# Performance work log

Measured on AMD Instinct MI355X. Metric: run time of the kernel, lower is better.

## Reference

```python
import jax, jax.numpy as jnp
import numpy as np

B, T, D = 2, 2048, 2048
H, KV, HD = 16, 8, 128
N_REP = H // KV
EPS = 1e-6
ROPE_THETA = 5e6
K_MASK = float(jnp.finfo(jnp.bfloat16).min)


def setup_inputs() -> dict:
    key = jax.random.key(0)
    ks = jax.random.split(key, 8)
    x = jax.random.normal(ks[0], (B, T, D), dtype=jnp.float32)
    wq = jax.random.normal(ks[1], (D, H * HD), dtype=jnp.float32) * 0.02
    wk = jax.random.normal(ks[2], (D, KV * HD), dtype=jnp.float32) * 0.02
    wv = jax.random.normal(ks[3], (D, KV * HD), dtype=jnp.float32) * 0.02
    wo = jax.random.normal(ks[4], (H * HD, D), dtype=jnp.float32) * 0.02
    qn_w = jnp.ones((HD,), dtype=jnp.float32)
    kn_w = jnp.ones((HD,), dtype=jnp.float32)
    # real rotary angles: [T, HD//2] -> broadcast to [B, T, HD//2]
    pos = jnp.arange(T, dtype=jnp.float32)
    inv_freq = 1.0 / (ROPE_THETA ** (jnp.arange(0, HD, 2, dtype=jnp.float32) / HD))
    ang = pos[:, None] * inv_freq[None, :]
    sin = jnp.broadcast_to(jnp.sin(ang)[None], (B, T, HD // 2))
    cos = jnp.broadcast_to(jnp.cos(ang)[None], (B, T, HD // 2))
    # causal mask [B, 1, T, T]
    causal = jnp.tril(jnp.ones((T, T), dtype=jnp.bool_))
    mask = jnp.broadcast_to(causal[None, None], (B, 1, T, T))
    k_cache = jnp.zeros((B, T, KV, HD), dtype=jnp.float32)
    v_cache = jnp.zeros((B, T, KV, HD), dtype=jnp.float32)
    return {"x": x, "wq": wq, "wk": wk, "wv": wv, "wo": wo,
            "qn_w": qn_w, "kn_w": kn_w, "sin": sin, "cos": cos,
            "mask": mask, "k_cache": k_cache, "v_cache": v_cache}


def _rms_norm(h, w):
    h32 = h.astype(jnp.float32)
    rms = jax.lax.rsqrt(jnp.mean(h32 * h32, axis=-1, keepdims=True) + EPS)
    return (h32 * rms * w).astype(h.dtype)


def _apply_rope(x, sin, cos):
    x1, x2 = x[..., : HD // 2], x[..., HD // 2:]
    s, c = sin[:, :, None, :], cos[:, :, None, :]  # [B,T,1,HD/2]
    return jnp.concatenate([x1 * c - x2 * s, x2 * c + x1 * s], axis=-1).astype(x.dtype)


def reference(x, wq, wk, wv, wo, qn_w, kn_w, sin, cos, mask, k_cache, v_cache):
    b, t, _ = x.shape
    q = _rms_norm((x @ wq).reshape(b, t, H, HD), qn_w)
    k = _rms_norm((x @ wk).reshape(b, t, KV, HD), kn_w)
    v = (x @ wv).reshape(b, t, KV, HD)
    q = _apply_rope(q, sin, cos)
    k = _apply_rope(k, sin, cos)
    # KV-cache update at cur_ind = 0 (prefill)
    k_cache = jax.lax.dynamic_update_slice(k_cache, k.astype(k_cache.dtype), (0, 0, 0, 0))
    v_cache = jax.lax.dynamic_update_slice(v_cache, v.astype(v_cache.dtype), (0, 0, 0, 0))
    # GQA repeat_kv: [B,S,KV,HD] -> [B,S,H,HD]
    kf = jnp.repeat(k_cache, N_REP, axis=2)
    vf = jnp.repeat(v_cache, N_REP, axis=2)
    scale = HD ** -0.5
    # [B,H,T,S]
    attn = jnp.einsum('bthd,bshd->bhts', q, kf) * scale
    attn = jnp.where(mask, attn, K_MASK)
    attn = jax.nn.softmax(attn.astype(jnp.float32), axis=-1).astype(q.dtype)
    out = jnp.einsum('bhts,bshd->bthd', attn, vf).reshape(b, t, H * HD)
    return out @ wo
```

## Files before the change

kernel.cpp:

```cpp
#include <hip/hip_runtime.h>
#include <hip/hip_bf16.h>
#include <stdint.h>

#define BB 2
#define TT 2048
#define DD 2048
#define HH 16
#define KVH 8
#define HDIM 128
#define BT (BB*TT)
#define NQKV (HH*HDIM + 2*KVH*HDIM)
#define TQ (TT/128)
#define ATT_SCALE 0.08838834764831845f
#define RMS_EPS 1e-6f

typedef __bf16 bf16;
typedef __bf16 bf16x8 __attribute__((ext_vector_type(8)));
typedef __bf16 bf16x4 __attribute__((ext_vector_type(4)));
typedef __bf16 bf16x2 __attribute__((ext_vector_type(2)));
typedef float  f32x4  __attribute__((ext_vector_type(4)));
typedef float  f32x16 __attribute__((ext_vector_type(16)));
typedef unsigned u32x4 __attribute__((ext_vector_type(4)));

__device__ __forceinline__ void gl_lds16(const void* g, const void* l) {
  __builtin_amdgcn_global_load_lds(
      (const __attribute__((address_space(1))) void*)(uintptr_t)g,
      (__attribute__((address_space(3))) void*)(uint32_t)(uintptr_t)l,
      16, 0, 0);
}

__device__ __forceinline__ unsigned pkbf(float lo, float hi) {
  bf16x2 t = { (bf16)lo, (bf16)hi };
  return __builtin_bit_cast(unsigned, t);
}

__global__ __launch_bounds__(256) void cast_bf16_k(const float* __restrict__ in,
                                                   bf16* __restrict__ out, int n4) {
  int i = blockIdx.x * blockDim.x + threadIdx.x;
  int stride = gridDim.x * blockDim.x;
  for (; i < n4; i += stride) {
    float4 v = ((const float4*)in)[i];
    bf16x4 o = { (bf16)v.x, (bf16)v.y, (bf16)v.z, (bf16)v.w };
    *(bf16x4*)(out + (size_t)i * 4) = o;
  }
}

__global__ __launch_bounds__(256) void transpose_cast_k(const float* __restrict__ in,
                                                        bf16* __restrict__ out,
                                                        int R, int C) {
  __shared__ float tile[32][33];
  int tx = threadIdx.x & 31, ty = threadIdx.x >> 5;
  int c0 = blockIdx.x * 32, r0 = blockIdx.y * 32;
#pragma unroll
  for (int i = 0; i < 4; ++i)
    tile[ty + 8*i][tx] = in[(size_t)(r0 + ty + 8*i) * C + c0 + tx];
  __syncthreads();
#pragma unroll
  for (int i = 0; i < 4; ++i)
    out[(size_t)(c0 + ty + 8*i) * R + r0 + tx] = (bf16)tile[tx][ty + 8*i];
}

__global__ __launch_bounds__(256) void transpose_v_k(const bf16* __restrict__ vb,
                                                     bf16* __restrict__ vbt) {
  __shared__ bf16 tile[32][33];
  int tx = threadIdx.x & 31, ty = threadIdx.x >> 5;
  int t0 = blockIdx.x * 32;
  int d0 = blockIdx.y * 32;
  int bk = blockIdx.z;
  int b = bk >> 3, kv = bk & 7;
#pragma unroll
  for (int i = 0; i < 4; ++i)
    tile[ty + 8*i][tx] = vb[(((size_t)(b*TT + t0 + ty + 8*i)) * KVH + kv) * HDIM + d0 + tx];
  __syncthreads();
#pragma unroll
  for (int i = 0; i < 4; ++i)
    vbt[(((size_t)bk) * HDIM + d0 + ty + 8*i) * TT + t0 + tx] = tile[tx][ty + 8*i];
}

template <int OUT_F32>
__global__ __launch_bounds__(256, 2)
void gemm_bt_k(const bf16* __restrict__ A, const bf16* __restrict__ Bt,
               void* __restrict__ Cout, int M, int N, int K) {
  __shared__ bf16 As[128 * 32];
  __shared__ bf16 Bs[128 * 32];
  const int tid = threadIdx.x;
  const int lane = tid & 63, wid = tid >> 6;
  const int lr = lane & 15, lq = lane >> 4;
  const int bm = blockIdx.y * 128, bn = blockIdx.x * 128;
  const int wr = wid >> 1, wc = wid & 1;
  const bf16* Ab = A + (size_t)bm * K;
  const bf16* Bb = Bt + (size_t)bn * K;
  f32x4 acc[4][4] = {};
  for (int k0 = 0; k0 < K; k0 += 32) {
#pragma unroll
    for (int r = 0; r < 2; ++r) {
      int ch = r * 256 + tid;
      int row = ch >> 2, c8 = ch & 3;
      const bf16* lbase = As + (size_t)(r * 256 + wid * 64) * 8;
      gl_lds16(Ab + (size_t)row * K + k0 + c8 * 8, lbase);
      const bf16* lbase2 = Bs + (size_t)(r * 256 + wid * 64) * 8;
      gl_lds16(Bb + (size_t)row * K + k0 + c8 * 8, lbase2);
    }
    __syncthreads();
    bf16x8 af[4], bfv[4];
#pragma unroll
    for (int m = 0; m < 4; ++m)
      af[m] = *(const bf16x8*)&As[(wr * 64 + m * 16 + lr) * 32 + lq * 8];
#pragma unroll
    for (int n = 0; n < 4; ++n)
      bfv[n] = *(const bf16x8*)&Bs[(wc * 64 + n * 16 + lr) * 32 + lq * 8];
#pragma unroll
    for (int m = 0; m < 4; ++m)
#pragma unroll
      for (int n = 0; n < 4; ++n)
        acc[m][n] = __builtin_amdgcn_mfma_f32_16x16x32_bf16(af[m], bfv[n], acc[m][n], 0, 0, 0);
    __syncthreads();
  }
#pragma unroll
  for (int m = 0; m < 4; ++m)
#pragma unroll
    for (int n = 0; n < 4; ++n)
#pragma unroll
      for (int r = 0; r < 4; ++r) {
        int row = bm + wr * 64 + m * 16 + lq * 4 + r;
        int col = bn + wc * 64 + n * 16 + lr;
        if (OUT_F32) ((float*)Cout)[(size_t)row * N + col] = acc[m][n][r];
        else         ((bf16*)Cout)[(size_t)row * N + col] = (bf16)acc[m][n][r];
      }
}

template <int OUT_F32>
__global__ __launch_bounds__(512, 2)
void gemm256_k(const bf16* __restrict__ A, const bf16* __restrict__ Bt,
               void* __restrict__ Cout, int M, int N, int K) {
  __shared__ bf16 S[2 * 2 * 2 * 128 * 64];
  const int tid = threadIdx.x, lane = tid & 63, wid = tid >> 6;
  const int lr = lane & 15, lq = lane >> 4;
  const int wrow = wid >> 1, wcol = wid & 1;

  const int nwg = gridDim.x;
  const int o = blockIdx.x;
  const int ns = (o & 7) * (nwg >> 3) + (o >> 3);
  const int GX = N >> 8;
  const int by = ns / GX, bx = ns % GX;

  const int NT = K >> 6;
  const bf16* Ab = A + (size_t)(by * 256) * K;
  const bf16* Bb = Bt + (size_t)(bx * 256) * K;

  const int srow = tid >> 3;
  const size_t soff = (size_t)srow * K + (((tid & 7) ^ (srow & 7)) * 8);
  const int ldst0 = wid * 512;

  auto STAGE = [&](int op, int h, int t_) {
    int tc = t_ < NT ? t_ : NT - 1;
    const bf16* src = (op ? Bb : Ab) + soff + (size_t)(h * 128) * K + tc * 64;
    bf16* dst = S + ((((((t_ & 1) << 1) | op) << 1) | h) << 13) + ldst0;
#pragma unroll
    for (int i = 0; i < 2; ++i)
      gl_lds16(src + (size_t)(i * 64) * K, dst + i * 4096);
  };

  bf16x8 af[2][2][2];
  bf16x8 bfr[4][2];
  f32x4 acc[4][2][4] = {};

  auto LOAD_A = [&](int buf) {
#pragma unroll
    for (int mh = 0; mh < 2; ++mh) {
      const bf16* base = S + (((buf << 2) | mh) << 13);
#pragma unroll
      for (int m = 0; m < 2; ++m) {
        int ra = wrow * 32 + m * 16 + lr;
#pragma unroll
        for (int ks = 0; ks < 2; ++ks)
          af[mh][m][ks] = *(const bf16x8*)(base + ra * 64 + (((ks * 4 + lq) ^ (ra & 7)) * 8));
      }
    }
  };
  auto LOAD_B = [&](int buf, int nh) {
    const bf16* base = S + (((buf << 2) | 2 | nh) << 13);
#pragma unroll
    for (int n = 0; n < 4; ++n) {
      int rb = wcol * 64 + n * 16 + lr;
#pragma unroll
      for (int ks = 0; ks < 2; ++ks)
        bfr[n][ks] = *(const bf16x8*)(base + rb * 64 + (((ks * 4 + lq) ^ (rb & 7)) * 8));
    }
  };
  auto MFMA_Q = [&](int qd, int mh) {
#pragma unroll
    for (int m = 0; m < 2; ++m)
#pragma unroll
      for (int n = 0; n < 4; ++n)
#pragma unroll
        for (int ks = 0; ks < 2; ++ks)
          acc[qd][m][n] = __builtin_amdgcn_mfma_f32_16x16x32_bf16(
              af[mh][m][ks], bfr[n][ks], acc[qd][m][n], 0, 0, 0);
  };

  STAGE(0, 0, 0); STAGE(0, 1, 0); STAGE(1, 0, 0); STAGE(1, 1, 0);
  STAGE(0, 0, 1); STAGE(0, 1, 1); STAGE(1, 0, 1);
  asm volatile("s_waitcnt vmcnt(6)" ::: "memory");
  __builtin_amdgcn_sched_barrier(0);
  __builtin_amdgcn_s_barrier();

  for (int t = 0; t < NT; ++t) {
    const int buf = t & 1;
    LOAD_A(buf);
    LOAD_B(buf, 0);
    STAGE(1, 1, t + 1);
    __builtin_amdgcn_s_barrier();
    asm volatile("s_waitcnt lgkmcnt(0)" ::: "memory");
    __builtin_amdgcn_sched_barrier(0);
    __builtin_amdgcn_s_setprio(1);
    MFMA_Q(0, 0);
    __builtin_amdgcn_s_setprio(0);
    __builtin_amdgcn_sched_barrier(0);
    __builtin_amdgcn_s_barrier();
    STAGE(0, 0, t + 2);
    __builtin_amdgcn_s_barrier();
    __builtin_amdgcn_s_setprio(1);
    MFMA_Q(1, 1);
    __builtin_amdgcn_s_setprio(0);
    __builtin_amdgcn_sched_barrier(0);
    __builtin_amdgcn_s_barrier();
    LOAD_B(buf, 1);
    STAGE(0, 1, t + 2);
    __builtin_amdgcn_s_barrier();
    asm volatile("s_waitcnt lgkmcnt(0)" ::: "memory");
    __builtin_amdgcn_sched_barrier(0);
    __builtin_amdgcn_s_setprio(1);
    MFMA_Q(2, 1);
    __builtin_amdgcn_s_setprio(0);
    __builtin_amdgcn_sched_barrier(0);
    __builtin_amdgcn_s_barrier();
    STAGE(1, 0, t + 2);
    asm volatile("s_waitcnt vmcnt(6)" ::: "memory");
    __builtin_amdgcn_sched_barrier(0);
    __builtin_amdgcn_s_barrier();
    __builtin_amdgcn_s_setprio(1);
    MFMA_Q(3, 0);
    __builtin_amdgcn_s_setprio(0);
    __builtin_amdgcn_sched_barrier(0);
    __builtin_amdgcn_s_barrier();
  }

#pragma unroll
  for (int qd = 0; qd < 4; ++qd) {
    const int mh = (qd == 1 || qd == 2) ? 1 : 0;
    const int nh = (qd >= 2) ? 1 : 0;
#pragma unroll
    for (int m = 0; m < 2; ++m)
#pragma unroll
      for (int n = 0; n < 4; ++n)
#pragma unroll
        for (int j = 0; j < 4; ++j) {
          int row = by * 256 + mh * 128 + wrow * 32 + m * 16 + lq * 4 + j;
          int col = bx * 256 + nh * 128 + wcol * 64 + n * 16 + lr;
          if (OUT_F32) ((float*)Cout)[(size_t)row * N + col] = acc[qd][m][n][j];
          else         ((bf16*)Cout)[(size_t)row * N + col] = (bf16)acc[qd][m][n][j];
        }
  }
}

__global__ __launch_bounds__(256) void norm_rope_k(const bf16* __restrict__ qkv,
                                                   const float* __restrict__ qn_w,
                                                   const float* __restrict__ kn_w,
                                                   const float* __restrict__ sinb,
                                                   const float* __restrict__ cosb,
                                                   bf16* __restrict__ qro,
                                                   bf16* __restrict__ kro,
                                                   bf16* __restrict__ vo) {
  const int bt = blockIdx.x;
  const int b = bt >> 11, t = bt & 2047;
  const int tid = threadIdx.x, lane = tid & 63, wid = tid >> 6;
  const bf16* row = qkv + (size_t)bt * NQKV;
  const float sv = sinb[bt * 64 + lane];
  const float cv = cosb[bt * 64 + lane];
  for (int it = 0; it < 8; ++it) {
    int hv = it * 4 + wid;
    int off = (hv < 16) ? hv * 128 : (hv < 24) ? 2048 + (hv - 16) * 128 : 3072 + (hv - 24) * 128;
    float e0 = (float)row[off + lane];
    float e1 = (float)row[off + 64 + lane];
    if (hv >= 24) {
      bf16* dst = vo + (size_t)bt * (KVH * HDIM) + (hv - 24) * 128;
      dst[lane] = (bf16)e0;
      dst[64 + lane] = (bf16)e1;
    } else {
      float ss = e0 * e0 + e1 * e1;
#pragma unroll
      for (int o = 32; o >= 1; o >>= 1) ss += __shfl_xor(ss, o, 64);
      float rms = rsqrtf(ss * (1.0f / 128.0f) + RMS_EPS);
      const float* wn = (hv < 16) ? qn_w : kn_w;
      float n0 = e0 * rms * wn[lane];
      float n1 = e1 * rms * wn[lane + 64];
      float o0 = n0 * cv - n1 * sv;
      float o1 = n1 * cv + n0 * sv;
      if (hv < 16) {
        bf16* dst = qro + (size_t)bt * (HH * HDIM) + hv * 128;
        dst[lane] = (bf16)o0; dst[64 + lane] = (bf16)o1;
      } else {
        bf16* dst = kro + (((size_t)b * KVH + (hv - 16)) * TT + t) * HDIM;
        dst[lane] = (bf16)o0; dst[64 + lane] = (bf16)o1;
      }
    }
  }
}

__global__ __launch_bounds__(256, 2)
void attn7_k(const bf16* __restrict__ qr, const bf16* __restrict__ kr2,
             const bf16* __restrict__ vbt, bf16* __restrict__ ao) {
  __shared__ bf16 Ks[2][64 * 128];
  __shared__ bf16 Vs[2][128 * 64];
  const int tid = threadIdx.x, lane = tid & 63, wid = tid >> 6;
  const int l31 = lane & 31, hi = lane >> 5;
  const int h = blockIdx.y, b = blockIdx.z;
  const int qt = (b & 1) ? (TQ - 1 - blockIdx.x) : blockIdx.x;
  const int kvh = h >> 1;
  const int q0w = qt * 128 + wid * 32;
  const int qg = q0w + l31;
  const int nt = 2 * qt + 2;

  const bf16* Kbase = kr2 + ((size_t)(b * KVH + kvh)) * TT * HDIM;
  const bf16* Vbase = vbt + ((size_t)(b * KVH + kvh)) * ((size_t)HDIM * TT);

  auto STAGE = [&](int bufi, int kt) {
#pragma unroll
    for (int i = 0; i < 4; ++i) {
      int u = i * 256 + tid;
      int krow = u >> 4, kcc = u & 15;
      gl_lds16(Kbase + (size_t)(kt * 64 + krow) * HDIM + ((kcc ^ (krow & 15)) * 8),
               &Ks[bufi][(i * 256 + wid * 64) * 8]);
      int vrow = u >> 3, vcc = u & 7;
      gl_lds16(Vbase + (size_t)vrow * TT + kt * 64 + ((vcc ^ (vrow & 7)) * 8),
               &Vs[bufi][(i * 256 + wid * 64) * 8]);
    }
  };

  bf16x8 qf[8];
  const bf16* qrow = &qr[(((size_t)(b * TT + qg)) * HH + h) * HDIM];
#pragma unroll
  for (int ks = 0; ks < 8; ++ks)
    qf[ks] = *(const bf16x8*)(qrow + ks * 16 + hi * 8);

  f32x16 accO[4] = {};
  float m = -INFINITY, lsum = 0.f;
  const float SC2 = ATT_SCALE * 1.4426950408889634f;

  int buf = 0;
  STAGE(0, 0);
  __syncthreads();

  for (int kt = 0; kt < nt; ++kt) {
    if (kt + 1 < nt) STAGE(buf ^ 1, kt + 1);

    if (kt * 64 <= q0w + 31) {
      const char* Kb = (const char*)&Ks[buf][0];
      const char* Vb = (const char*)&Vs[buf][0];
      const bool do1 = (kt * 64 + 32) <= (q0w + 31);
      const bool domask = (kt * 64 + 63) > q0w;

      f32x16 sacc[2];
#pragma unroll
      for (int ct = 0; ct < 2; ++ct) {
        if (ct == 0 || do1) {
#pragma unroll
          for (int j = 0; j < 16; ++j) sacc[ct][j] = 0.f;
          int krow = ct * 32 + l31;
#pragma unroll
          for (int ks = 0; ks < 8; ++ks) {
            bf16x8 kf = *(const bf16x8*)(Kb + krow * 256 + (((2 * ks + hi) ^ (krow & 15)) * 16));
            sacc[ct] = __builtin_amdgcn_mfma_f32_32x32x16_bf16(kf, qf[ks], sacc[ct], 0, 0, 0);
          }
        }
      }

      float p[2][16];
      float pmx = -INFINITY;
#pragma unroll
      for (int ct = 0; ct < 2; ++ct) {
        if (ct == 0 || do1) {
          if (domask) {
            int lim = qg - (kt * 64 + ct * 32 + 4 * hi);
#pragma unroll
            for (int r = 0; r < 16; ++r) {
              const int crow0 = (r & 3) + 8 * (r >> 2);
              float v = sacc[ct][r] * SC2;
              v = (crow0 <= lim) ? v : -INFINITY;
              p[ct][r] = v;
              pmx = fmaxf(pmx, v);
            }
          } else {
#pragma unroll
            for (int r = 0; r < 16; ++r) {
              float v = sacc[ct][r] * SC2;
              p[ct][r] = v;
              pmx = fmaxf(pmx, v);
            }
          }
        }
      }
      pmx = fmaxf(pmx, __shfl_xor(pmx, 32, 64));

      if (__any(pmx > m + 11.54f)) {
        float mnew = fmaxf(m, pmx);
        float alpha = exp2f(m - mnew);
        m = mnew;
        lsum *= alpha;
        int ai = __builtin_bit_cast(int, alpha);
#pragma unroll
        for (int r = 0; r < 16; ++r) {
          const int crow = (r & 3) + 8 * (r >> 2) + 4 * hi;
          float av = __builtin_bit_cast(float, __builtin_amdgcn_ds_bpermute(crow << 2, ai));
#pragma unroll
          for (int n = 0; n < 4; ++n) accO[n][r] *= av;
        }
      }

      float rsum = 0.f;
#pragma unroll
      for (int ct = 0; ct < 2; ++ct)
        if (ct == 0 || do1)
#pragma unroll
          for (int r = 0; r < 16; ++r) {
            float e = exp2f(p[ct][r] - m);
            p[ct][r] = e;
            rsum += e;
          }
      rsum += __shfl_xor(rsum, 32, 64);
      lsum += rsum;

      bf16x8 pa[4];
#pragma unroll
      for (int ct = 0; ct < 2; ++ct) {
        if (ct == 0 || do1) {
          unsigned W[8];
#pragma unroll
          for (int mi = 0; mi < 8; ++mi)
            W[mi] = pkbf(p[ct][2 * mi], p[ct][2 * mi + 1]);
#pragma unroll
          for (int a = 0; a < 2; ++a) {
            unsigned s0 = __shfl_xor(W[4 * a + 0], 32, 64);
            unsigned s1 = __shfl_xor(W[4 * a + 1], 32, 64);
            unsigned s2 = __shfl_xor(W[4 * a + 2], 32, 64);
            unsigned s3 = __shfl_xor(W[4 * a + 3], 32, 64);
            u32x4 wv;
            wv[0] = hi ? s2 : W[4 * a + 0];
            wv[1] = hi ? s3 : W[4 * a + 1];
            wv[2] = hi ? W[4 * a + 2] : s0;
            wv[3] = hi ? W[4 * a + 3] : s1;
            pa[ct * 2 + a] = __builtin_bit_cast(bf16x8, wv);
          }
        }
      }

#pragma unroll
      for (int n = 0; n < 4; ++n) {
        int vrow = n * 32 + l31;
#pragma unroll
        for (int ks = 0; ks < 4; ++ks) {
          if (ks < 2 || do1) {
            bf16x8 vf = *(const bf16x8*)(Vb + vrow * 128 + (((2 * ks + hi) ^ (vrow & 7)) * 16));
            accO[n] = __builtin_amdgcn_mfma_f32_32x32x16_bf16(pa[ks], vf, accO[n], 0, 0, 0);
          }
        }
      }
    }

    __syncthreads();
    buf ^= 1;
  }

  float inv = 1.0f / lsum;
  int ii = __builtin_bit_cast(int, inv);
#pragma unroll
  for (int n = 0; n < 4; ++n)
#pragma unroll
    for (int r = 0; r < 16; ++r) {
      const int crow = (r & 3) + 8 * (r >> 2) + 4 * hi;
      float av = __builtin_bit_cast(float, __builtin_amdgcn_ds_bpermute(crow << 2, ii));
      size_t idx = (((size_t)(b * TT + q0w + crow)) * HH + h) * HDIM + n * 32 + l31;
      ao[idx] = (bf16)(accO[n][r] * av);
    }
}

extern "C" void kernel_launch(void* const* d_in, const int* in_sizes, int n_in,
                              void* d_out, int out_size, void* d_ws, size_t ws_size,
                              hipStream_t stream) {
  const float* x    = (const float*)d_in[0];
  const float* wq   = (const float*)d_in[1];
  const float* wk   = (const float*)d_in[2];
  const float* wv   = (const float*)d_in[3];
  const float* wo   = (const float*)d_in[4];
  const float* qn_w = (const float*)d_in[5];
  const float* kn_w = (const float*)d_in[6];
  const float* sinb = (const float*)d_in[7];
  const float* cosb = (const float*)d_in[8];
  float* out = (float*)d_out;

  char* ws = (char*)d_ws;
  size_t off = 0;
  auto alloc = [&](size_t bytes) {
    char* p = ws + off;
    off += (bytes + 255) & ~(size_t)255;
    return p;
  };
  bf16* xb  = (bf16*)alloc((size_t)BT * DD * 2);
  bf16* Wt  = (bf16*)alloc((size_t)NQKV * DD * 2);
  bf16* Wot = (bf16*)alloc((size_t)DD * DD * 2);
  bf16* qkv = (bf16*)alloc((size_t)BT * NQKV * 2);
  bf16* kro = (bf16*)alloc((size_t)BT * KVH * HDIM * 2);
  bf16* vb  = (bf16*)alloc((size_t)BT * KVH * HDIM * 2);
  bf16* vbt = (bf16*)alloc((size_t)BT * KVH * HDIM * 2);
  bf16* qro = Wt;
  bf16* aob = xb;
  (void)ws_size; (void)in_sizes; (void)n_in; (void)out_size;

  cast_bf16_k<<<2048, 256, 0, stream>>>(x, xb, BT * DD / 4);
  transpose_cast_k<<<dim3(2048 / 32, 2048 / 32), 256, 0, stream>>>(wq, Wt, 2048, 2048);
  transpose_cast_k<<<dim3(1024 / 32, 2048 / 32), 256, 0, stream>>>(wk, Wt + (size_t)2048 * 2048, 2048, 1024);
  transpose_cast_k<<<dim3(1024 / 32, 2048 / 32), 256, 0, stream>>>(wv, Wt + (size_t)3072 * 2048, 2048, 1024);
  transpose_cast_k<<<dim3(2048 / 32, 2048 / 32), 256, 0, stream>>>(wo, Wot, 2048, 2048);

  gemm256_k<0><<<dim3((BT / 256) * (NQKV / 256)), 512, 0, stream>>>(xb, Wt, qkv, BT, NQKV, DD);

  norm_rope_k<<<BT, 256, 0, stream>>>(qkv, qn_w, kn_w, sinb, cosb, qro, kro, vb);
  transpose_v_k<<<dim3(TT / 32, HDIM / 32, BB * KVH), 256, 0, stream>>>(vb, vbt);

  attn7_k<<<dim3(TQ, HH, BB), 256, 0, stream>>>(qro, kro, vbt, aob);

  gemm_bt_k<1><<<dim3(DD / 128, BT / 128), 256, 0, stream>>>(aob, Wot, out, BT, DD, DD);
}
```

Baseline: 234.6 us.

## Fuse prep casts into one launch, add pipelined 256x128 output GEMM, simplify attention

Merges the x cast and four weight transpose-casts into a single prep_k launch, which removes per-launch overhead. Replaces the simple 128x128 output-projection GEMM with a 256x128 tile kernel that uses double-buffered direct-to-LDS staging, swizzled LDS layout and MFMA priority hints, to improve reuse and overlap memory with compute. In the attention kernel it drops the do1 branch that skipped the second 32-key half on diagonal tiles. Masking keeps results correct, but a few diagonal tiles now do extra MFMA work in exchange for less branching.

```diff
diff --git a/kernel.cpp b/kernel.cpp
--- a/kernel.cpp
+++ b/kernel.cpp
@@ -34,23 +34,36 @@
   return __builtin_bit_cast(unsigned, t);
 }
 
-__global__ __launch_bounds__(256) void cast_bf16_k(const float* __restrict__ in,
-                                                   bf16* __restrict__ out, int n4) {
-  int i = blockIdx.x * blockDim.x + threadIdx.x;
-  int stride = gridDim.x * blockDim.x;
-  for (; i < n4; i += stride) {
-    float4 v = ((const float4*)in)[i];
-    bf16x4 o = { (bf16)v.x, (bf16)v.y, (bf16)v.z, (bf16)v.w };
-    *(bf16x4*)(out + (size_t)i * 4) = o;
+__global__ __launch_bounds__(256) void prep_k(const float* __restrict__ x,
+                                              const float* __restrict__ wq,
+                                              const float* __restrict__ wk,
+                                              const float* __restrict__ wv,
+                                              const float* __restrict__ wo,
+                                              bf16* __restrict__ xb,
+                                              bf16* __restrict__ Wt,
+                                              bf16* __restrict__ Wot) {
+  const int z = blockIdx.z;
+  if (z == 0) {
+    int id = (blockIdx.y * 64 + blockIdx.x) * 256 + threadIdx.x;
+#pragma unroll
+    for (int i = 0; i < 2; ++i) {
+      int idx = id + i * 1048576;
+      float4 v = ((const float4*)x)[idx];
+      bf16x4 o4 = { (bf16)v.x, (bf16)v.y, (bf16)v.z, (bf16)v.w };
+      *(bf16x4*)(xb + (size_t)idx * 4) = o4;
+    }
+    return;
   }
-}
-
-__global__ __launch_bounds__(256) void transpose_cast_k(const float* __restrict__ in,
-                                                        bf16* __restrict__ out,
-                                                        int R, int C) {
+  const float* in; bf16* out; int C;
+  const int R = 2048;
+  if (z == 1)      { in = wq; out = Wt;                          C = 2048; }
+  else if (z == 2) { in = wk; out = Wt + (size_t)2048 * 2048;    C = 1024; }
+  else if (z == 3) { in = wv; out = Wt + (size_t)3072 * 2048;    C = 1024; }
+  else             { in = wo; out = Wot;                         C = 2048; }
+  int c0 = blockIdx.x * 32, r0 = blockIdx.y * 32;
+  if (c0 >= C) return;
   __shared__ float tile[32][33];
   int tx = threadIdx.x & 31, ty = threadIdx.x >> 5;
-  int c0 = blockIdx.x * 32, r0 = blockIdx.y * 32;
 #pragma unroll
   for (int i = 0; i < 4; ++i)
     tile[ty + 8*i][tx] = in[(size_t)(r0 + ty + 8*i) * C + c0 + tx];
@@ -78,58 +91,6 @@
 }
 
 template <int OUT_F32>
-__global__ __launch_bounds__(256, 2)
-void gemm_bt_k(const bf16* __restrict__ A, const bf16* __restrict__ Bt,
-               void* __restrict__ Cout, int M, int N, int K) {
-  __shared__ bf16 As[128 * 32];
-  __shared__ bf16 Bs[128 * 32];
-  const int tid = threadIdx.x;
-  const int lane = tid & 63, wid = tid >> 6;
-  const int lr = lane & 15, lq = lane >> 4;
-  const int bm = blockIdx.y * 128, bn = blockIdx.x * 128;
-  const int wr = wid >> 1, wc = wid & 1;
-  const bf16* Ab = A + (size_t)bm * K;
-  const bf16* Bb = Bt + (size_t)bn * K;
-  f32x4 acc[4][4] = {};
-  for (int k0 = 0; k0 < K; k0 += 32) {
-#pragma unroll
-    for (int r = 0; r < 2; ++r) {
-      int ch = r * 256 + tid;
-      int row = ch >> 2, c8 = ch & 3;
-      const bf16* lbase = As + (size_t)(r * 256 + wid * 64) * 8;
-      gl_lds16(Ab + (size_t)row * K + k0 + c8 * 8, lbase);
-      const bf16* lbase2 = Bs + (size_t)(r * 256 + wid * 64) * 8;
-      gl_lds16(Bb + (size_t)row * K + k0 + c8 * 8, lbase2);
-    }
-    __syncthreads();
-    bf16x8 af[4], bfv[4];
-#pragma unroll
-    for (int m = 0; m < 4; ++m)
-      af[m] = *(const bf16x8*)&As[(wr * 64 + m * 16 + lr) * 32 + lq * 8];
-#pragma unroll
-    for (int n = 0; n < 4; ++n)
-      bfv[n] = *(const bf16x8*)&Bs[(wc * 64 + n * 16 + lr) * 32 + lq * 8];
-#pragma unroll
-    for (int m = 0; m < 4; ++m)
-#pragma unroll
-      for (int n = 0; n < 4; ++n)
-        acc[m][n] = __builtin_amdgcn_mfma_f32_16x16x32_bf16(af[m], bfv[n], acc[m][n], 0, 0, 0);
-    __syncthreads();
-  }
-#pragma unroll
-  for (int m = 0; m < 4; ++m)
-#pragma unroll
-    for (int n = 0; n < 4; ++n)
-#pragma unroll
-      for (int r = 0; r < 4; ++r) {
-        int row = bm + wr * 64 + m * 16 + lq * 4 + r;
-        int col = bn + wc * 64 + n * 16 + lr;
-        if (OUT_F32) ((float*)Cout)[(size_t)row * N + col] = acc[m][n][r];
-        else         ((bf16*)Cout)[(size_t)row * N + col] = (bf16)acc[m][n][r];
-      }
-}
-
-template <int OUT_F32>
 __global__ __launch_bounds__(512, 2)
 void gemm256_k(const bf16* __restrict__ A, const bf16* __restrict__ Bt,
                void* __restrict__ Cout, int M, int N, int K) {
@@ -262,6 +223,118 @@
           else         ((bf16*)Cout)[(size_t)row * N + col] = (bf16)acc[qd][m][n][j];
         }
   }
+}
+
+template <int OUT_F32>
+__global__ __launch_bounds__(512, 1)
+void gemm256x128_k(const bf16* __restrict__ A, const bf16* __restrict__ Bt,
+                   void* __restrict__ Cout, int M, int N, int K) {
+  __shared__ bf16 S[2 * 3 * 128 * 64];
+  const int tid = threadIdx.x, lane = tid & 63, wid = tid >> 6;
+  const int lr = lane & 15, lq = lane >> 4;
+  const int wrow = wid >> 1, wcol = wid & 1;
+
+  const int nwg = gridDim.x;
+  const int o = blockIdx.x;
+  const int ns = (o & 7) * (nwg >> 3) + (o >> 3);
+  const int GX = N >> 7;
+  const int by = ns / GX, bx = ns % GX;
+
+  const int NT = K >> 6;
+  const bf16* Ab = A + (size_t)(by * 256) * K;
+  const bf16* Bb = Bt + (size_t)(bx * 128) * K;
+
+  const int srow = tid >> 3;
+  const size_t soff = (size_t)srow * K + (((tid & 7) ^ (srow & 7)) * 8);
+  const int ldst0 = wid * 512;
+
+  auto STAGE = [&](int sec, int t_) {
+    int tc = t_ < NT ? t_ : NT - 1;
+    const bf16* src = (sec == 2 ? Bb : Ab + (size_t)(sec * 128) * K) + soff + tc * 64;
+    bf16* dst = S + ((t_ & 1) * 3 + sec) * 8192 + ldst0;
+#pragma unroll
+    for (int i = 0; i < 2; ++i)
+      gl_lds16(src + (size_t)(i * 64) * K, dst + i * 4096);
+  };
+
+  bf16x8 af[2][2][2];
+  bf16x8 bfr[4][2];
+  f32x4 acc[2][2][4] = {};
+
+  auto LOAD_A = [&](int buf) {
+#pragma unroll
+    for (int mh = 0; mh < 2; ++mh) {
+      const bf16* base = S + (buf * 3 + mh) * 8192;
+#pragma unroll
+      for (int m = 0; m < 2; ++m) {
+        int ra = wrow * 32 + m * 16 + lr;
+#pragma unroll
+        for (int ks = 0; ks < 2; ++ks)
+          af[mh][m][ks] = *(const bf16x8*)(base + ra * 64 + (((ks * 4 + lq) ^ (ra & 7)) * 8));
+      }
+    }
+  };
+  auto LOAD_B = [&](int buf) {
+    const bf16* base = S + (buf * 3 + 2) * 8192;
+#pragma unroll
+    for (int n = 0; n < 4; ++n) {
+      int rb = wcol * 64 + n * 16 + lr;
+#pragma unroll
+      for (int ks = 0; ks < 2; ++ks)
+        bfr[n][ks] = *(const bf16x8*)(base + rb * 64 + (((ks * 4 + lq) ^ (rb & 7)) * 8));
+    }
+  };
+  auto MFMA_H = [&](int mh) {
+#pragma unroll
+    for (int m = 0; m < 2; ++m)
+#pragma unroll
+      for (int n = 0; n < 4; ++n)
+#pragma unroll
+        for (int ks = 0; ks < 2; ++ks)
+          acc[mh][m][n] = __builtin_amdgcn_mfma_f32_16x16x32_bf16(
+              af[mh][m][ks], bfr[n][ks], acc[mh][m][n], 0, 0, 0);
+  };
+
+  STAGE(0, 0); STAGE(1, 0); STAGE(2, 0);
+  STAGE(0, 1); STAGE(1, 1); STAGE(2, 1);
+  asm volatile("s_waitcnt vmcnt(6)" ::: "memory");
+  __builtin_amdgcn_sched_barrier(0);
+  __builtin_amdgcn_s_barrier();
+
+  for (int t = 0; t < NT; ++t) {
+    const int buf = t & 1;
+    LOAD_A(buf);
+    LOAD_B(buf);
+    asm volatile("s_waitcnt lgkmcnt(0)" ::: "memory");
+    __builtin_amdgcn_sched_barrier(0);
+    __builtin_amdgcn_s_setprio(1);
+    MFMA_H(0);
+    __builtin_amdgcn_s_setprio(0);
+    __builtin_amdgcn_sched_barrier(0);
+    __builtin_amdgcn_s_barrier();
+    STAGE(0, t + 2); STAGE(1, t + 2); STAGE(2, t + 2);
+    asm volatile("s_waitcnt vmcnt(6)" ::: "memory");
+    __builtin_amdgcn_sched_barrier(0);
+    __builtin_amdgcn_s_barrier();
+    __builtin_amdgcn_s_setprio(1);
+    MFMA_H(1);
+    __builtin_amdgcn_s_setprio(0);
+    __builtin_amdgcn_sched_barrier(0);
+  }
+
+#pragma unroll
+  for (int mh = 0; mh < 2; ++mh)
+#pragma unroll
+    for (int m = 0; m < 2; ++m)
+#pragma unroll
+      for (int n = 0; n < 4; ++n)
+#pragma unroll
+        for (int j = 0; j < 4; ++j) {
+          int row = by * 256 + mh * 128 + wrow * 32 + m * 16 + lq * 4 + j;
+          int col = bx * 128 + wcol * 64 + n * 16 + lr;
+          if (OUT_F32) ((float*)Cout)[(size_t)row * N + col] = acc[mh][m][n][j];
+          else         ((bf16*)Cout)[(size_t)row * N + col] = (bf16)acc[mh][m][n][j];
+        }
 }
 
 __global__ __launch_bounds__(256) void norm_rope_k(const bf16* __restrict__ qkv,
@@ -309,7 +382,7 @@
 }
 
 __global__ __launch_bounds__(256, 2)
-void attn7_k(const bf16* __restrict__ qr, const bf16* __restrict__ kr2,
+void attn8_k(const bf16* __restrict__ qr, const bf16* __restrict__ kr2,
              const bf16* __restrict__ vbt, bf16* __restrict__ ao) {
   __shared__ bf16 Ks[2][64 * 128];
   __shared__ bf16 Vs[2][128 * 64];
@@ -358,48 +431,45 @@
     if (kt * 64 <= q0w + 31) {
       const char* Kb = (const char*)&Ks[buf][0];
       const char* Vb = (const char*)&Vs[buf][0];
-      const bool do1 = (kt * 64 + 32) <= (q0w + 31);
       const bool domask = (kt * 64 + 63) > q0w;
 
       f32x16 sacc[2];
 #pragma unroll
       for (int ct = 0; ct < 2; ++ct) {
-        if (ct == 0 || do1) {
-#pragma unroll
-          for (int j = 0; j < 16; ++j) sacc[ct][j] = 0.f;
-          int krow = ct * 32 + l31;
-#pragma unroll
-          for (int ks = 0; ks < 8; ++ks) {
-            bf16x8 kf = *(const bf16x8*)(Kb + krow * 256 + (((2 * ks + hi) ^ (krow & 15)) * 16));
-            sacc[ct] = __builtin_amdgcn_mfma_f32_32x32x16_bf16(kf, qf[ks], sacc[ct], 0, 0, 0);
-          }
+#pragma unroll
+        for (int j = 0; j < 16; ++j) sacc[ct][j] = 0.f;
+        int krow = ct * 32 + l31;
+#pragma unroll
+        for (int ks = 0; ks < 8; ++ks) {
+          bf16x8 kf = *(const bf16x8*)(Kb + krow * 256 + (((2 * ks + hi) ^ (krow & 15)) * 16));
+          sacc[ct] = __builtin_amdgcn_mfma_f32_32x32x16_bf16(kf, qf[ks], sacc[ct], 0, 0, 0);
         }
       }
 
       float p[2][16];
       float pmx = -INFINITY;
-#pragma unroll
-      for (int ct = 0; ct < 2; ++ct) {
-        if (ct == 0 || do1) {
-          if (domask) {
-            int lim = qg - (kt * 64 + ct * 32 + 4 * hi);
-#pragma unroll
-            for (int r = 0; r < 16; ++r) {
-              const int crow0 = (r & 3) + 8 * (r >> 2);
-              float v = sacc[ct][r] * SC2;
-              v = (crow0 <= lim) ? v : -INFINITY;
-              p[ct][r] = v;
-              pmx = fmaxf(pmx, v);
-            }
-          } else {
-#pragma unroll
-            for (int r = 0; r < 16; ++r) {
-              float v = sacc[ct][r] * SC2;
-              p[ct][r] = v;
-              pmx = fmaxf(pmx, v);
-            }
+      if (domask) {
+#pragma unroll
+        for (int ct = 0; ct < 2; ++ct) {
+          int lim = qg - (kt * 64 + ct * 32 + 4 * hi);
+#pragma unroll
+          for (int r = 0; r < 16; ++r) {
+            const int crow0 = (r & 3) + 8 * (r >> 2);
+            float v = sacc[ct][r] * SC2;
+            v = (crow0 <= lim) ? v : -INFINITY;
+            p[ct][r] = v;
+            pmx = fmaxf(pmx, v);
           }
         }
+      } else {
+#pragma unroll
+        for (int ct = 0; ct < 2; ++ct)
+#pragma unroll
+          for (int r = 0; r < 16; ++r) {
+            float v = sacc[ct][r] * SC2;
+            p[ct][r] = v;
+            pmx = fmaxf(pmx, v);
+          }
       }
       pmx = fmaxf(pmx, __shfl_xor(pmx, 32, 64));
 
@@ -421,37 +491,34 @@
       float rsum = 0.f;
 #pragma unroll
       for (int ct = 0; ct < 2; ++ct)
-        if (ct == 0 || do1)
-#pragma unroll
-          for (int r = 0; r < 16; ++r) {
-            float e = exp2f(p[ct][r] - m);
-            p[ct][r] = e;
-            rsum += e;
-          }
+#pragma unroll
+        for (int r = 0; r < 16; ++r) {
+          float e = exp2f(p[ct][r] - m);
+          p[ct][r] = e;
+          rsum += e;
+        }
       rsum += __shfl_xor(rsum, 32, 64);
       lsum += rsum;
 
       bf16x8 pa[4];
 #pragma unroll
       for (int ct = 0; ct < 2; ++ct) {
-        if (ct == 0 || do1) {
-          unsigned W[8];
-#pragma unroll
-          for (int mi = 0; mi < 8; ++mi)
-            W[mi] = pkbf(p[ct][2 * mi], p[ct][2 * mi + 1]);
-#pragma unroll
-          for (int a = 0; a < 2; ++a) {
-            unsigned s0 = __shfl_xor(W[4 * a + 0], 32, 64);
-            unsigned s1 = __shfl_xor(W[4 * a + 1], 32, 64);
-            unsigned s2 = __shfl_xor(W[4 * a + 2], 32, 64);
-            unsigned s3 = __shfl_xor(W[4 * a + 3], 32, 64);
-            u32x4 wv;
-            wv[0] = hi ? s2 : W[4 * a + 0];
-            wv[1] = hi ? s3 : W[4 * a + 1];
-            wv[2] = hi ? W[4 * a + 2] : s0;
-            wv[3] = hi ? W[4 * a + 3] : s1;
-            pa[ct * 2 + a] = __builtin_bit_cast(bf16x8, wv);
-          }
+        unsigned W[8];
+#pragma unroll
+        for (int mi = 0; mi < 8; ++mi)
+          W[mi] = pkbf(p[ct][2 * mi], p[ct][2 * mi + 1]);
+#pragma unroll
+        for (int a = 0; a < 2; ++a) {
+          unsigned s0 = __shfl_xor(W[4 * a + 0], 32, 64);
+          unsigned s1 = __shfl_xor(W[4 * a + 1], 32, 64);
+          unsigned s2 = __shfl_xor(W[4 * a + 2], 32, 64);
+          unsigned s3 = __shfl_xor(W[4 * a + 3], 32, 64);
+          u32x4 wv;
+          wv[0] = hi ? s2 : W[4 * a + 0];
+          wv[1] = hi ? s3 : W[4 * a + 1];
+          wv[2] = hi ? W[4 * a + 2] : s0;
+          wv[3] = hi ? W[4 * a + 3] : s1;
+          pa[ct * 2 + a] = __builtin_bit_cast(bf16x8, wv);
         }
       }
 
@@ -460,10 +527,8 @@
         int vrow = n * 32 + l31;
 #pragma unroll
         for (int ks = 0; ks < 4; ++ks) {
-          if (ks < 2 || do1) {
-            bf16x8 vf = *(const bf16x8*)(Vb + vrow * 128 + (((2 * ks + hi) ^ (vrow & 7)) * 16));
-            accO[n] = __builtin_amdgcn_mfma_f32_32x32x16_bf16(pa[ks], vf, accO[n], 0, 0, 0);
-          }
+          bf16x8 vf = *(const bf16x8*)(Vb + vrow * 128 + (((2 * ks + hi) ^ (vrow & 7)) * 16));
+          accO[n] = __builtin_amdgcn_mfma_f32_32x32x16_bf16(pa[ks], vf, accO[n], 0, 0, 0);
         }
       }
     }
@@ -517,18 +582,14 @@
   bf16* aob = xb;
   (void)ws_size; (void)in_sizes; (void)n_in; (void)out_size;
 
-  cast_bf16_k<<<2048, 256, 0, stream>>>(x, xb, BT * DD / 4);
-  transpose_cast_k<<<dim3(2048 / 32, 2048 / 32), 256, 0, stream>>>(wq, Wt, 2048, 2048);
-  transpose_cast_k<<<dim3(1024 / 32, 2048 / 32), 256, 0, stream>>>(wk, Wt + (size_t)2048 * 2048, 2048, 1024);
-  transpose_cast_k<<<dim3(1024 / 32, 2048 / 32), 256, 0, stream>>>(wv, Wt + (size_t)3072 * 2048, 2048, 1024);
-  transpose_cast_k<<<dim3(2048 / 32, 2048 / 32), 256, 0, stream>>>(wo, Wot, 2048, 2048);
+  prep_k<<<dim3(64, 64, 5), 256, 0, stream>>>(x, wq, wk, wv, wo, xb, Wt, Wot);
 
   gemm256_k<0><<<dim3((BT / 256) * (NQKV / 256)), 512, 0, stream>>>(xb, Wt, qkv, BT, NQKV, DD);
 
   norm_rope_k<<<BT, 256, 0, stream>>>(qkv, qn_w, kn_w, sinb, cosb, qro, kro, vb);
   transpose_v_k<<<dim3(TT / 32, HDIM / 32, BB * KVH), 256, 0, stream>>>(vb, vbt);
 
-  attn7_k<<<dim3(TQ, HH, BB), 256, 0, stream>>>(qro, kro, vbt, aob);
-
-  gemm_bt_k<1><<<dim3(DD / 128, BT / 128), 256, 0, stream>>>(aob, Wot, out, BT, DD, DD);
-}
+  attn8_k<<<dim3(TQ, HH, BB), 256, 0, stream>>>(qro, kro, vbt, aob);
+
+  gemm256x128_k<1><<<dim3((BT / 256) * (DD / 128)), 512, 0, stream>>>(aob, Wot, out, BT, DD, DD);
+}
```

New measurement: 209.3 us. -10.8%, faster.
